# Kernel optimization log

Hardware: AMD Instinct MI355X
Metric: run time of the kernel (lower is better)

## Reference

```python
import jax, jax.numpy as jnp
import numpy as np

K = 7  # kernel_size

def setup_inputs() -> dict:
    key = jax.random.key(0)
    k1, k2, k3 = jax.random.split(key, 3)
    X = jax.random.normal(k1, (32, 256, 64, 64), dtype=jnp.float32)
    # PyTorch Conv2d default init: uniform(-b, b), b = 1/sqrt(fan_in), fan_in = 2*7*7
    bound = 1.0 / np.sqrt(2 * K * K)
    conv_w = jax.random.uniform(k2, (1, 2, K, K), dtype=jnp.float32, minval=-bound, maxval=bound)
    conv_b = jax.random.uniform(k3, (1,), dtype=jnp.float32, minval=-bound, maxval=bound)
    return {"X": X, "conv_w": conv_w, "conv_b": conv_b}

def reference(X, conv_w, conv_b):
    # channel-wise max and mean pooling -> [B, 2, H, W]
    max_pool = jnp.max(X, axis=1, keepdims=True)
    avg_pool = jnp.mean(X, axis=1, keepdims=True)
    pool_out = jnp.concatenate([max_pool, avg_pool], axis=1)
    # 2 -> 1 channel 7x7 conv, stride 1, padding 3 (SAME for odd K)
    out = jax.lax.conv_general_dilated(
        pool_out, conv_w,
        window_strides=(1, 1),
        padding=[(K // 2, K // 2), (K // 2, K // 2)],
        dimension_numbers=("NCHW", "OIHW", "NCHW"),
    ) + conv_b[None, :, None, None]
    gate = jax.nn.sigmoid(out)  # [B, 1, H, W]
    return gate * X
```

## Files before the change

kernel.cpp:

```cpp
#include <hip/hip_runtime.h>
#include <math.h>

#define Bn 32
#define Cn 256
#define Hn 64
#define Wn 64
#define HWn (Hn * Wn)
#define CHWn (Cn * HWn)

__global__ __launch_bounds__(256) void pool_kernel(const float* __restrict__ X,
                                                   float* __restrict__ maxp,
                                                   float* __restrict__ avgp) {
    const int tid   = threadIdx.x;
    const int w4    = tid & 15;
    const int c_sub = tid >> 4;
    const int b     = blockIdx.x >> 6;
    const int h     = blockIdx.x & 63;

    const float4* Xb = (const float4*)(X + (size_t)b * CHWn + (size_t)h * Wn) + w4;

    float4 mx = make_float4(-INFINITY, -INFINITY, -INFINITY, -INFINITY);
    float4 sm = make_float4(0.f, 0.f, 0.f, 0.f);
    #pragma unroll
    for (int k = 0; k < 16; ++k) {
        const int c = c_sub * 16 + k;
        float4 v = Xb[(size_t)c * (HWn / 4)];
        mx.x = fmaxf(mx.x, v.x); mx.y = fmaxf(mx.y, v.y);
        mx.z = fmaxf(mx.z, v.z); mx.w = fmaxf(mx.w, v.w);
        sm.x += v.x; sm.y += v.y; sm.z += v.z; sm.w += v.w;
    }

    __shared__ float4 smax[256];
    __shared__ float4 ssum[256];
    smax[tid] = mx;
    ssum[tid] = sm;
    __syncthreads();

    #pragma unroll
    for (int s = 128; s >= 16; s >>= 1) {
        if (tid < s) {
            float4 a = smax[tid], c = smax[tid + s];
            a.x = fmaxf(a.x, c.x); a.y = fmaxf(a.y, c.y);
            a.z = fmaxf(a.z, c.z); a.w = fmaxf(a.w, c.w);
            smax[tid] = a;
            float4 p = ssum[tid], q = ssum[tid + s];
            p.x += q.x; p.y += q.y; p.z += q.z; p.w += q.w;
            ssum[tid] = p;
        }
        __syncthreads();
    }

    if (tid < 16) {
        float4 m = smax[tid];
        float4 s4 = ssum[tid];
        const float inv = 1.0f / (float)Cn;
        float4 a = make_float4(s4.x * inv, s4.y * inv, s4.z * inv, s4.w * inv);
        const int o = b * (HWn / 4) + h * 16 + tid;
        ((float4*)maxp)[o] = m;
        ((float4*)avgp)[o] = a;
    }
}

__global__ __launch_bounds__(256) void conv_kernel(const float* __restrict__ maxp,
                                                   const float* __restrict__ avgp,
                                                   const float* __restrict__ wgt,
                                                   const float* __restrict__ bias,
                                                   float* __restrict__ gate) {
    __shared__ float ws[98];
    const int tid = threadIdx.x;
    if (tid < 98) ws[tid] = wgt[tid];
    __syncthreads();

    const int idx = blockIdx.x * 256 + tid;
    const int b = idx >> 12;
    const int y = (idx >> 6) & 63;
    const int x = idx & 63;

    const float* mp = maxp + b * HWn;
    const float* ap = avgp + b * HWn;

    float acc = bias[0];
    #pragma unroll
    for (int i = 0; i < 7; ++i) {
        const int yy = y + i - 3;
        if (yy < 0 || yy >= Hn) continue;
        #pragma unroll
        for (int j = 0; j < 7; ++j) {
            const int xx = x + j - 3;
            if (xx < 0 || xx >= Wn) continue;
            const int o = yy * Wn + xx;
            acc += ws[i * 7 + j] * mp[o] + ws[49 + i * 7 + j] * ap[o];
        }
    }
    gate[idx] = 1.0f / (1.0f + expf(-acc));
}

__global__ __launch_bounds__(256) void scale_kernel(const float* __restrict__ X,
                                                    const float* __restrict__ gate,
                                                    float* __restrict__ out) {
    const float4* X4 = (const float4*)X;
    const float4* G4 = (const float4*)gate;
    float4* O4 = (float4*)out;
    const int total4 = Bn * CHWn / 4;
    const int step = gridDim.x * blockDim.x;
    for (int v = blockIdx.x * blockDim.x + threadIdx.x; v < total4; v += step) {
        const int hw4 = v & 1023;
        const int b   = v >> 18;
        float4 g = G4[b * 1024 + hw4];
        float4 x = X4[v];
        O4[v] = make_float4(g.x * x.x, g.y * x.y, g.z * x.z, g.w * x.w);
    }
}

extern "C" void kernel_launch(void* const* d_in, const int* in_sizes, int n_in,
                              void* d_out, int out_size, void* d_ws, size_t ws_size,
                              hipStream_t stream) {
    const float* X      = (const float*)d_in[0];
    const float* conv_w = (const float*)d_in[1];
    const float* conv_b = (const float*)d_in[2];
    float* out = (float*)d_out;

    float* maxp = (float*)d_ws;
    float* avgp = maxp + Bn * HWn;
    float* gate = avgp + Bn * HWn;

    pool_kernel<<<Bn * Hn, 256, 0, stream>>>(X, maxp, avgp);

    conv_kernel<<<(Bn * HWn) / 256, 256, 0, stream>>>(maxp, avgp, conv_w, conv_b, gate);

    scale_kernel<<<2048, 256, 0, stream>>>(X, gate, out);
}
```

Measured before the change: 77.13 us.

## Fuse conv+sigmoid gate into scale kernel with nontemporal loads/stores

```diff
diff --git a/kernel.cpp b/kernel.cpp
--- a/kernel.cpp
+++ b/kernel.cpp
@@ -8,6 +8,8 @@
 #define HWn (Hn * Wn)
 #define CHWn (Cn * HWn)
 
+typedef float f32x4 __attribute__((ext_vector_type(4)));
+
 __global__ __launch_bounds__(256) void pool_kernel(const float* __restrict__ X,
                                                    float* __restrict__ maxp,
                                                    float* __restrict__ avgp) {
@@ -17,21 +19,21 @@
     const int b     = blockIdx.x >> 6;
     const int h     = blockIdx.x & 63;
 
-    const float4* Xb = (const float4*)(X + (size_t)b * CHWn + (size_t)h * Wn) + w4;
+    const f32x4* Xb = (const f32x4*)(X + (size_t)b * CHWn + (size_t)h * Wn) + w4;
 
-    float4 mx = make_float4(-INFINITY, -INFINITY, -INFINITY, -INFINITY);
-    float4 sm = make_float4(0.f, 0.f, 0.f, 0.f);
+    f32x4 mx = { -INFINITY, -INFINITY, -INFINITY, -INFINITY };
+    f32x4 sm = { 0.f, 0.f, 0.f, 0.f };
     #pragma unroll
     for (int k = 0; k < 16; ++k) {
         const int c = c_sub * 16 + k;
-        float4 v = Xb[(size_t)c * (HWn / 4)];
+        f32x4 v = Xb[(size_t)c * (HWn / 4)];
         mx.x = fmaxf(mx.x, v.x); mx.y = fmaxf(mx.y, v.y);
         mx.z = fmaxf(mx.z, v.z); mx.w = fmaxf(mx.w, v.w);
-        sm.x += v.x; sm.y += v.y; sm.z += v.z; sm.w += v.w;
+        sm += v;
     }
 
-    __shared__ float4 smax[256];
-    __shared__ float4 ssum[256];
+    __shared__ f32x4 smax[256];
+    __shared__ f32x4 ssum[256];
     smax[tid] = mx;
     ssum[tid] = sm;
     __syncthreads();
@@ -39,76 +41,75 @@
     #pragma unroll
     for (int s = 128; s >= 16; s >>= 1) {
         if (tid < s) {
-            float4 a = smax[tid], c = smax[tid + s];
+            f32x4 a = smax[tid], c = smax[tid + s];
             a.x = fmaxf(a.x, c.x); a.y = fmaxf(a.y, c.y);
             a.z = fmaxf(a.z, c.z); a.w = fmaxf(a.w, c.w);
             smax[tid] = a;
-            float4 p = ssum[tid], q = ssum[tid + s];
-            p.x += q.x; p.y += q.y; p.z += q.z; p.w += q.w;
-            ssum[tid] = p;
+            ssum[tid] += ssum[tid + s];
         }
         __syncthreads();
     }
 
     if (tid < 16) {
-        float4 m = smax[tid];
-        float4 s4 = ssum[tid];
-        const float inv = 1.0f / (float)Cn;
-        float4 a = make_float4(s4.x * inv, s4.y * inv, s4.z * inv, s4.w * inv);
+        f32x4 m = smax[tid];
+        f32x4 a = ssum[tid] * (1.0f / (float)Cn);
         const int o = b * (HWn / 4) + h * 16 + tid;
-        ((float4*)maxp)[o] = m;
-        ((float4*)avgp)[o] = a;
+        ((f32x4*)maxp)[o] = m;
+        ((f32x4*)avgp)[o] = a;
     }
 }
 
-__global__ __launch_bounds__(256) void conv_kernel(const float* __restrict__ maxp,
-                                                   const float* __restrict__ avgp,
-                                                   const float* __restrict__ wgt,
-                                                   const float* __restrict__ bias,
-                                                   float* __restrict__ gate) {
+__global__ __launch_bounds__(256) void conv_scale_kernel(const float* __restrict__ X,
+                                                         const float* __restrict__ maxp,
+                                                         const float* __restrict__ avgp,
+                                                         const float* __restrict__ wgt,
+                                                         const float* __restrict__ bias,
+                                                         float* __restrict__ out) {
     __shared__ float ws[98];
+    __shared__ float gate[64];
+
     const int tid = threadIdx.x;
+    const int b = blockIdx.x >> 6;
+    const int h = blockIdx.x & 63;
+
     if (tid < 98) ws[tid] = wgt[tid];
     __syncthreads();
 
-    const int idx = blockIdx.x * 256 + tid;
-    const int b = idx >> 12;
-    const int y = (idx >> 6) & 63;
-    const int x = idx & 63;
+    if (tid < 64) {
+        const int x = tid;
+        const float* mp = maxp + b * HWn;
+        const float* ap = avgp + b * HWn;
+        float acc = bias[0];
+        #pragma unroll
+        for (int i = 0; i < 7; ++i) {
+            const int yy = h + i - 3;
+            if (yy < 0 || yy >= Hn) continue;
+            #pragma unroll
+            for (int j = 0; j < 7; ++j) {
+                const int xx = x + j - 3;
+                if (xx < 0 || xx >= Wn) continue;
+                const int o = yy * Wn + xx;
+                acc += ws[i * 7 + j] * mp[o] + ws[49 + i * 7 + j] * ap[o];
+            }
+        }
+        gate[x] = 1.0f / (1.0f + expf(-acc));
+    }
+    __syncthreads();
 
-    const float* mp = maxp + b * HWn;
-    const float* ap = avgp + b * HWn;
+    const int w4 = tid & 15;
+    const int c0 = tid >> 4;
+    const f32x4 g = ((const f32x4*)gate)[w4];
 
-    float acc = bias[0];
+    const f32x4* X4 = (const f32x4*)(X   + (size_t)b * CHWn + (size_t)h * Wn) + w4;
+    f32x4*       O4 = (f32x4*)      (out + (size_t)b * CHWn + (size_t)h * Wn) + w4;
+
     #pragma unroll
-    for (int i = 0; i < 7; ++i) {
-        const int yy = y + i - 3;
-        if (yy < 0 || yy >= Hn) continue;
-        #pragma unroll
-        for (int j = 0; j < 7; ++j) {
-            const int xx = x + j - 3;
-            if (xx < 0 || xx >= Wn) continue;
-            const int o = yy * Wn + xx;
-            acc += ws[i * 7 + j] * mp[o] + ws[49 + i * 7 + j] * ap[o];
-        }
-    }
-    gate[idx] = 1.0f / (1.0f + expf(-acc));
-}
-
-__global__ __launch_bounds__(256) void scale_kernel(const float* __restrict__ X,
-                                                    const float* __restrict__ gate,
-                                                    float* __restrict__ out) {
-    const float4* X4 = (const float4*)X;
-    const float4* G4 = (const float4*)gate;
-    float4* O4 = (float4*)out;
-    const int total4 = Bn * CHWn / 4;
-    const int step = gridDim.x * blockDim.x;
-    for (int v = blockIdx.x * blockDim.x + threadIdx.x; v < total4; v += step) {
-        const int hw4 = v & 1023;
-        const int b   = v >> 18;
-        float4 g = G4[b * 1024 + hw4];
-        float4 x = X4[v];
-        O4[v] = make_float4(g.x * x.x, g.y * x.y, g.z * x.z, g.w * x.w);
+    for (int k = 0; k < 16; ++k) {
+        const int c = k * 16 + c0;
+        const size_t off = (size_t)c * (HWn / 4);
+        f32x4 v = __builtin_nontemporal_load(X4 + off);
+        v *= g;
+        __builtin_nontemporal_store(v, O4 + off);
     }
 }
 
@@ -122,11 +123,8 @@
 
     float* maxp = (float*)d_ws;
     float* avgp = maxp + Bn * HWn;
-    float* gate = avgp + Bn * HWn;
 
     pool_kernel<<<Bn * Hn, 256, 0, stream>>>(X, maxp, avgp);
 
-    conv_kernel<<<(Bn * HWn) / 256, 256, 0, stream>>>(maxp, avgp, conv_w, conv_b, gate);
-
-    scale_kernel<<<2048, 256, 0, stream>>>(X, gate, out);
+    conv_scale_kernel<<<Bn * Hn, 256, 0, stream>>>(X, maxp, avgp, conv_w, conv_b, out);
 }
```

Result: faster. 73.73 us (-4.4%).
